# Kernel tuning notes

Hardware: AMD Instinct MI355X
Metric: run time of the kernel (lower is better)

The kernel has to match this reference:

```python
import jax, jax.numpy as jnp
import numpy as np

HIDDEN = 1024
JOINTS = 21
IN_DIM = JOINTS * 3  # 63
BATCH = 64
SEQ = 512


def setup_inputs() -> dict:
    key = jax.random.key(0)
    ks = jax.random.split(key, 11)
    s = 0.02
    f32 = jnp.float32
    return {
        "real_seq": jax.random.normal(ks[0], (BATCH, SEQ, IN_DIM), f32),
        # PyTorch nn.GRU params (gates ordered r, z, n)
        "W_ih": jax.random.normal(ks[1], (3 * HIDDEN, IN_DIM), f32) * s,
        "W_hh": jax.random.normal(ks[2], (3 * HIDDEN, HIDDEN), f32) * s,
        "b_ih": jax.random.normal(ks[3], (3 * HIDDEN,), f32) * s,
        "b_hh": jax.random.normal(ks[4], (3 * HIDDEN,), f32) * s,
        # projector MLP (no nonlinearities in the original)
        "W1": jax.random.normal(ks[5], (HIDDEN, HIDDEN), f32) * s,
        "b1": jax.random.normal(ks[6], (HIDDEN,), f32) * s,
        "W2": jax.random.normal(ks[7], (HIDDEN, HIDDEN), f32) * s,
        "b2": jax.random.normal(ks[8], (HIDDEN,), f32) * s,
        "W3": jax.random.normal(ks[9], (IN_DIM, HIDDEN), f32) * s,
        "b3": jax.random.normal(ks[10], (IN_DIM,), f32) * s,
        "condition_length": 5,
        "ground_truth_length": 5,
    }


def _condition_list(seq_len, condition_length, ground_truth_length):
    gt = np.ones((100, ground_truth_length))
    co = np.zeros((100, condition_length))
    return np.concatenate((gt, co), 1).reshape(-1)[:seq_len]


def reference(real_seq, W_ih, W_hh, b_ih, b_hh, W1, b1, W2, b2, W3, b3,
              condition_length, ground_truth_length):
    B, T, D = real_seq.shape
    H = W_hh.shape[1]
    cond = jnp.asarray(_condition_list(T, condition_length, ground_truth_length),
                       dtype=real_seq.dtype)  # [T], static 1/0 teacher-forcing pattern

    h0 = jnp.zeros((B, H), real_seq.dtype)
    o0 = jnp.zeros((B, D), real_seq.dtype)
    xs = (jnp.transpose(real_seq, (1, 0, 2)), cond)  # time-major

    def step(carry, x):
        h, out = carry
        xt, c = x
        inp = jnp.where(c > 0.5, xt, out)  # teacher-forcing switch
        gi = inp @ W_ih.T + b_ih           # [B, 3H]
        gh = h @ W_hh.T + b_hh             # [B, 3H]
        i_r, i_z, i_n = jnp.split(gi, 3, axis=-1)
        h_r, h_z, h_n = jnp.split(gh, 3, axis=-1)
        r = jax.nn.sigmoid(i_r + h_r)
        z = jax.nn.sigmoid(i_z + h_z)
        n = jnp.tanh(i_n + r * h_n)
        h_new = (1.0 - z) * n + z * h
        lin = (h_new @ W1.T + b1) @ W2.T + b2
        out_new = inp + lin @ W3.T + b3    # residual velocities
        return (h_new, out_new), out_new

    _, outs = jax.lax.scan(step, (h0, o0), xs)  # outs: [T, B, D]
    return jnp.transpose(outs, (1, 0, 2)).reshape(B, T, D // 3, 3)
```

## Files before the change

kernel.cpp:

```cpp
#include <hip/hip_runtime.h>
#include <hip/hip_bf16.h>


#define HIDDEN 1024
#define INDIM  63
#define TSEQ   512
#define MB     16
#define NGRP   4
#define HWORDS 512

typedef __attribute__((ext_vector_type(8))) short bfrag8;
typedef __attribute__((ext_vector_type(4))) float ffrag4;
typedef unsigned long long ull;

#define MFMA_B16(a, b, c) __builtin_amdgcn_mfma_f32_16x16x32_bf16((a), (b), (c), 0, 0, 0)

__device__ __forceinline__ short f2bf(float x) {
  __hip_bfloat16 b = __float2bfloat16(x);
  return __builtin_bit_cast(short, b);
}
__device__ __forceinline__ float bf2f(short s) {
  unsigned u = ((unsigned)(unsigned short)s) << 16;
  return __builtin_bit_cast(float, u);
}


__global__ void k_t1(const float* __restrict__ W2, const float* __restrict__ b1,
                     const float* __restrict__ b2, float* __restrict__ t1) {
  const int w = threadIdx.x >> 6, lane = threadIdx.x & 63;
  const int o = blockIdx.x * 4 + w;
  if (o >= HIDDEN) return;
  const float* row = W2 + (size_t)o * HIDDEN;
  float s = 0.f;
  for (int k = lane; k < HIDDEN; k += 64) s += row[k] * b1[k];
  for (int off = 32; off; off >>= 1) s += __shfl_down(s, off, 64);
  if (lane == 0) t1[o] = s + b2[o];
}

__global__ void k_bp(const float* __restrict__ W3, const float* __restrict__ t1,
                     const float* __restrict__ b3, float* __restrict__ bp) {
  const int w = threadIdx.x >> 6, lane = threadIdx.x & 63;
  for (int d = w; d < INDIM; d += 4) {
    const float* row = W3 + (size_t)d * HIDDEN;
    float s = 0.f;
    for (int k = lane; k < HIDDEN; k += 64) s += row[k] * t1[k];
    for (int off = 32; off; off >>= 1) s += __shfl_down(s, off, 64);
    if (lane == 0) bp[d] = s + b3[d];
  }
}

__global__ void k_gemm(const float* __restrict__ A, const float* __restrict__ B,
                       float* __restrict__ C, int M, int N, int K) {
  __shared__ float As[16][17], Bs[16][17];
  const int tx = threadIdx.x, ty = threadIdx.y;
  const int row = blockIdx.y * 16 + ty;
  const int col = blockIdx.x * 16 + tx;
  float acc = 0.f;
  for (int k0 = 0; k0 < K; k0 += 16) {
    As[ty][tx] = (row < M) ? A[(size_t)row * K + k0 + tx] : 0.f;
    Bs[ty][tx] = B[(size_t)(k0 + ty) * N + col];
    __syncthreads();
#pragma unroll
    for (int kk = 0; kk < 16; ++kk) acc += As[ty][kk] * Bs[kk][tx];
    __syncthreads();
  }
  if (row < M && col < N) C[(size_t)row * N + col] = acc;
}


__global__ __launch_bounds__(256, 1) void k_main(
    const float* __restrict__ X,
    const float* __restrict__ W_ih, const float* __restrict__ W_hh,
    const float* __restrict__ b_ih, const float* __restrict__ b_hh,
    const float* __restrict__ WpF, const float* __restrict__ bpF,
    const int* __restrict__ pCL, const int* __restrict__ pGT,
    ull* __restrict__ hb, float* __restrict__ OUT) {
  __shared__ short h_st[MB][HIDDEN + 8];
  __shared__ short inp_bf[MB][88];
  __shared__ float inp_f[MB][68];
  __shared__ float gt_z[MB][16], gt_hn[MB][16];
  __shared__ float gt_ir[MB][16], gt_iz[MB][16], gt_in[MB][16];
  __shared__ short htmp[MB][16];
  __shared__ int pub_flag;

  const int tid = threadIdx.x;
  const int w = tid >> 6;
  const int lane = tid & 63;
  const int c = lane & 15;
  const int quad = lane >> 4;
  const int g = blockIdx.x >> 6;
  const int j = blockIdx.x & 63;

  const int gtv = pGT[0];
  int period = pCL[0] + gtv;
  if (period < 1) period = 1;

  bfrag8 wB[32];
  bfrag8 wp[32];
  if (w < 3) {
    const float* wr = W_hh + ((size_t)w * HIDDEN + (size_t)j * 16 + c) * HIDDEN;
#pragma unroll
    for (int ks = 0; ks < 32; ++ks) {
      const float* p = wr + ks * 32 + quad * 8;
      bfrag8 f;
#pragma unroll
      for (int e = 0; e < 8; ++e) f[e] = f2bf(p[e]);
      wB[ks] = f;
    }
  } else {
#pragma unroll
    for (int gate = 0; gate < 3; ++gate) {
      const float* wr = W_ih + ((size_t)gate * HIDDEN + (size_t)j * 16 + c) * INDIM;
#pragma unroll
      for (int ks = 0; ks < 2; ++ks) {
        bfrag8 f;
#pragma unroll
        for (int e = 0; e < 8; ++e) {
          int k = ks * 32 + quad * 8 + e;
          f[e] = (k < INDIM) ? f2bf(wr[k]) : (short)0;
        }
        wB[gate * 2 + ks] = f;
      }
    }
  }
  const int dd = 16 * w + c;
  {
    const float* wr = WpF + (size_t)dd * HIDDEN;
#pragma unroll
    for (int ks = 0; ks < 32; ++ks) {
      bfrag8 f;
#pragma unroll
      for (int e = 0; e < 8; ++e)
        f[e] = (dd < INDIM) ? f2bf(wr[ks * 32 + quad * 8 + e]) : (short)0;
      wp[ks] = f;
    }
  }

  float bias_g;
  if (w == 0)      bias_g = b_ih[j * 16 + c] + b_hh[j * 16 + c];
  else if (w == 1) bias_g = b_ih[HIDDEN + j * 16 + c] + b_hh[HIDDEN + j * 16 + c];
  else if (w == 2) bias_g = b_hh[2 * HIDDEN + j * 16 + c];
  else             bias_g = b_ih[2 * HIDDEN + j * 16 + c];
  const float bp_l = (dd < INDIM) ? bpF[dd] : 0.f;

  for (int i = tid; i < MB * (HIDDEN + 8); i += 256) ((short*)h_st)[i] = 0;
  for (int i = tid; i < MB * 88; i += 256) ((short*)inp_bf)[i] = 0;
  for (int i = tid; i < MB * 68; i += 256) ((float*)inp_f)[i] = 0.f;
  if (tid == 0) pub_flag = 0;

  ull* hb_g[2] = {hb + (size_t)g * MB * HWORDS,
                  hb + (size_t)(NGRP + g) * MB * HWORDS};

  for (int t = 0; t < TSEQ; ++t) {
    const unsigned tg = (unsigned)(t + 1);
    const bool teach = ((t % period) < gtv);
    if (teach) {
      const int row = tid >> 4, d0 = (tid & 15) * 4;
      const float* xr = X + ((size_t)(g * MB + row) * TSEQ + t) * INDIM;
#pragma unroll
      for (int e = 0; e < 4; ++e) {
        int d = d0 + e;
        float v = (d < INDIM) ? xr[d] : 0.f;
        inp_f[row][d] = v;
        inp_bf[row][d] = f2bf(v);
      }
    }
    __syncthreads();

    ffrag4 ghr;
    float hp[4];
    if (w < 3) {
      ffrag4 acc[4];
#pragma unroll
      for (int e = 0; e < 4; ++e) {
        acc[0][e] = bias_g; acc[1][e] = 0.f; acc[2][e] = 0.f; acc[3][e] = 0.f;
      }
#pragma unroll
      for (int ks = 0; ks < 32; ++ks) {
        const bfrag8 a = *(const bfrag8*)&h_st[c][ks * 32 + quad * 8];
        acc[ks & 3] = MFMA_B16(a, wB[ks], acc[ks & 3]);
      }
      ffrag4 gsum = acc[0] + acc[1] + acc[2] + acc[3];
      if (w == 1) {
#pragma unroll
        for (int i = 0; i < 4; ++i) gt_z[quad * 4 + i][c] = gsum[i];
      } else if (w == 2) {
#pragma unroll
        for (int i = 0; i < 4; ++i) gt_hn[quad * 4 + i][c] = gsum[i];
      } else {
        ghr = gsum;
#pragma unroll
        for (int i = 0; i < 4; ++i) hp[i] = bf2f(h_st[quad * 4 + i][j * 16 + c]);
      }
    } else {
      ffrag4 gir, giz, gin;
#pragma unroll
      for (int e = 0; e < 4; ++e) { gir[e] = 0.f; giz[e] = 0.f; gin[e] = bias_g; }
#pragma unroll
      for (int ks = 0; ks < 2; ++ks) {
        const bfrag8 a = *(const bfrag8*)&inp_bf[c][ks * 32 + quad * 8];
        gir = MFMA_B16(a, wB[0 + ks], gir);
        giz = MFMA_B16(a, wB[2 + ks], giz);
        gin = MFMA_B16(a, wB[4 + ks], gin);
      }
#pragma unroll
      for (int i = 0; i < 4; ++i) {
        gt_ir[quad * 4 + i][c] = gir[i];
        gt_iz[quad * 4 + i][c] = giz[i];
        gt_in[quad * 4 + i][c] = gin[i];
      }
    }
    __syncthreads();

    ull* hw = hb_g[t & 1];
    if (w == 0) {
#pragma unroll
      for (int i = 0; i < 4; ++i) {
        const int row = quad * 4 + i;
        float r = 1.f / (1.f + __expf(-(ghr[i] + gt_ir[row][c])));
        float z = 1.f / (1.f + __expf(-(gt_z[row][c] + gt_iz[row][c])));
        float n = tanhf(gt_in[row][c] + r * gt_hn[row][c]);
        htmp[row][c] = f2bf((1.f - z) * n + z * hp[i]);
      }
      asm volatile("" ::: "memory");
      const int r = lane >> 2, q4 = (lane & 3) * 4;
      unsigned lo0 = (unsigned)(unsigned short)htmp[r][q4 + 0] |
                     ((unsigned)(unsigned short)htmp[r][q4 + 1] << 16);
      unsigned lo1 = (unsigned)(unsigned short)htmp[r][q4 + 2] |
                     ((unsigned)(unsigned short)htmp[r][q4 + 3] << 16);
      ull w0v = ((ull)tg << 32) | lo0;
      ull w1v = ((ull)tg << 32) | lo1;
      ull* dst = hw + (size_t)r * HWORDS + 8 * j + (lane & 3) * 2;
      __hip_atomic_store(dst, w0v, __ATOMIC_RELAXED, __HIP_MEMORY_SCOPE_SYSTEM);
      __hip_atomic_store(dst + 1, w1v, __ATOMIC_RELAXED, __HIP_MEMORY_SCOPE_SYSTEM);
      asm volatile("" ::: "memory");
      if (lane == 0) *(volatile int*)&pub_flag = (int)tg;
    } else {
      while (*(volatile int*)&pub_flag < (int)tg) __builtin_amdgcn_s_sleep(1);
    }

    {
      ull v[32];
#pragma unroll
      for (int s = 0; s < 32; ++s)
        v[s] = __hip_atomic_load(&hw[tid + s * 256], __ATOMIC_RELAXED,
                                 __HIP_MEMORY_SCOPE_SYSTEM);
      bool bad = true;
      while (bad) {
        bad = false;
#pragma unroll
        for (int s = 0; s < 32; ++s) {
          if ((unsigned)(v[s] >> 32) != tg) {
            v[s] = __hip_atomic_load(&hw[tid + s * 256], __ATOMIC_RELAXED,
                                     __HIP_MEMORY_SCOPE_SYSTEM);
            bad = true;
          }
        }
      }
#pragma unroll
      for (int s = 0; s < 32; ++s) {
        const int widx = tid + s * 256;
        *(unsigned*)&h_st[widx >> 9][(widx & 511) * 2] = (unsigned)v[s];
      }
    }
    __syncthreads();

    const bool rep = (t + 1 < TSEQ) && !(((t + 1) % period) < gtv);
    if (rep || j == 0) {
      ffrag4 oa0, oa1;
#pragma unroll
      for (int e = 0; e < 4; ++e) { oa0[e] = bp_l; oa1[e] = 0.f; }
#pragma unroll
      for (int ks = 0; ks < 32; ++ks) {
        const bfrag8 a = *(const bfrag8*)&h_st[c][ks * 32 + quad * 8];
        if (ks & 1) oa1 = MFMA_B16(a, wp[ks], oa1);
        else        oa0 = MFMA_B16(a, wp[ks], oa0);
      }
      ffrag4 o = oa0 + oa1;
#pragma unroll
      for (int i = 0; i < 4; ++i) {
        const int row = quad * 4 + i;
        if (dd < INDIM) {
          float val = o[i] + inp_f[row][dd];
          if (j == 0) OUT[((size_t)(g * MB + row) * TSEQ + t) * INDIM + dd] = val;
          if (rep) { inp_f[row][dd] = val; inp_bf[row][dd] = f2bf(val); }
        } else if (rep) {
          inp_bf[row][dd] = 0;
        }
      }
    }
  }
}


extern "C" void kernel_launch(void* const* d_in, const int* in_sizes, int n_in,
                              void* d_out, int out_size, void* d_ws, size_t ws_size,
                              hipStream_t stream) {
  const float* X    = (const float*)d_in[0];
  const float* W_ih = (const float*)d_in[1];
  const float* W_hh = (const float*)d_in[2];
  const float* b_ih = (const float*)d_in[3];
  const float* b_hh = (const float*)d_in[4];
  const float* W1   = (const float*)d_in[5];
  const float* b1   = (const float*)d_in[6];
  const float* W2   = (const float*)d_in[7];
  const float* b2   = (const float*)d_in[8];
  const float* W3   = (const float*)d_in[9];
  const float* b3   = (const float*)d_in[10];
  const int* pCL    = (const int*)d_in[11];
  const int* pGT    = (const int*)d_in[12];
  float* OUT = (float*)d_out;

  char* ws = (char*)d_ws;
  float* bp = (float*)(ws + 1024);
  float* t1 = (float*)(ws + 2048);
  float* Wp = (float*)(ws + 8192);
  float* T2 = (float*)(ws + 270336);
  ull*   hb = (ull*)(ws + 270336);
  if (ws_size < 795 * 1024) return;

  k_t1<<<256, 256, 0, stream>>>(W2, b1, b2, t1);
  k_gemm<<<dim3(64, 4), dim3(16, 16), 0, stream>>>(W3, W2, T2, INDIM, HIDDEN, HIDDEN);
  k_gemm<<<dim3(64, 4), dim3(16, 16), 0, stream>>>(T2, W1, Wp, INDIM, HIDDEN, HIDDEN);
  k_bp<<<1, 256, 0, stream>>>(W3, t1, b3, bp);
  hipMemsetAsync(hb, 0, 2 * NGRP * MB * HWORDS * sizeof(ull), stream);
  k_main<<<256, 256, 0, stream>>>(X, W_ih, W_hh, b_ih, b_hh, Wp, bp, pCL, pGT, hb, OUT);
}
```

Baseline: 3.470 ms.

## Use per-block global ready flags and agent-scope atomics for hidden-state exchange

Swaps the per-step cross-block hidden-state handshake from system-scope tagged atomics to agent-scope ones. Producers now publish a per-block flag in global memory after a vmcnt wait, and consumers poll the group's 64 flags before reading the tagged words. The output-writing block rotates with the timestep instead of always being block 0. LDS scratch arrays are padded to reduce bank conflicts. The intent is to cut polling traffic and coherence cost on the serial recurrence critical path, at the cost of extra flag loads and reliance on relaxed ordering between data and flag stores.

```diff
diff --git a/kernel.cpp b/kernel.cpp
--- a/kernel.cpp
+++ b/kernel.cpp
@@ -74,14 +74,13 @@
     const float* __restrict__ b_ih, const float* __restrict__ b_hh,
     const float* __restrict__ WpF, const float* __restrict__ bpF,
     const int* __restrict__ pCL, const int* __restrict__ pGT,
-    ull* __restrict__ hb, float* __restrict__ OUT) {
+    ull* __restrict__ hb, int* __restrict__ fl, float* __restrict__ OUT) {
   __shared__ short h_st[MB][HIDDEN + 8];
   __shared__ short inp_bf[MB][88];
   __shared__ float inp_f[MB][68];
-  __shared__ float gt_z[MB][16], gt_hn[MB][16];
-  __shared__ float gt_ir[MB][16], gt_iz[MB][16], gt_in[MB][16];
-  __shared__ short htmp[MB][16];
-  __shared__ int pub_flag;
+  __shared__ float gt_z[MB][20], gt_hn[MB][20];
+  __shared__ float gt_ir[MB][20], gt_iz[MB][20], gt_in[MB][20];
+  __shared__ short htmp[MB][20];
 
   const int tid = threadIdx.x;
   const int w = tid >> 6;
@@ -146,10 +145,12 @@
   for (int i = tid; i < MB * (HIDDEN + 8); i += 256) ((short*)h_st)[i] = 0;
   for (int i = tid; i < MB * 88; i += 256) ((short*)inp_bf)[i] = 0;
   for (int i = tid; i < MB * 68; i += 256) ((float*)inp_f)[i] = 0.f;
-  if (tid == 0) pub_flag = 0;
 
   ull* hb_g[2] = {hb + (size_t)g * MB * HWORDS,
                   hb + (size_t)(NGRP + g) * MB * HWORDS};
+  int* fg = fl + g * 64;
+  const int fj1 = tid >> 3;
+  const int fj2 = fj1 + 32;
 
   for (int t = 0; t < TSEQ; ++t) {
     const unsigned tg = (unsigned)(t + 1);
@@ -231,20 +232,27 @@
       ull w0v = ((ull)tg << 32) | lo0;
       ull w1v = ((ull)tg << 32) | lo1;
       ull* dst = hw + (size_t)r * HWORDS + 8 * j + (lane & 3) * 2;
-      __hip_atomic_store(dst, w0v, __ATOMIC_RELAXED, __HIP_MEMORY_SCOPE_SYSTEM);
-      __hip_atomic_store(dst + 1, w1v, __ATOMIC_RELAXED, __HIP_MEMORY_SCOPE_SYSTEM);
-      asm volatile("" ::: "memory");
-      if (lane == 0) *(volatile int*)&pub_flag = (int)tg;
-    } else {
-      while (*(volatile int*)&pub_flag < (int)tg) __builtin_amdgcn_s_sleep(1);
+      __hip_atomic_store(dst, w0v, __ATOMIC_RELAXED, __HIP_MEMORY_SCOPE_AGENT);
+      __hip_atomic_store(dst + 1, w1v, __ATOMIC_RELAXED, __HIP_MEMORY_SCOPE_AGENT);
+      asm volatile("s_waitcnt vmcnt(0)" ::: "memory");
+      if (lane == 0)
+        __hip_atomic_store(&fg[j], (int)tg, __ATOMIC_RELAXED,
+                           __HIP_MEMORY_SCOPE_AGENT);
     }
 
     {
+      while (__hip_atomic_load(&fg[fj1], __ATOMIC_RELAXED,
+                               __HIP_MEMORY_SCOPE_AGENT) < (int)tg)
+        __builtin_amdgcn_s_sleep(1);
+      while (__hip_atomic_load(&fg[fj2], __ATOMIC_RELAXED,
+                               __HIP_MEMORY_SCOPE_AGENT) < (int)tg)
+        __builtin_amdgcn_s_sleep(1);
+
       ull v[32];
 #pragma unroll
       for (int s = 0; s < 32; ++s)
         v[s] = __hip_atomic_load(&hw[tid + s * 256], __ATOMIC_RELAXED,
-                                 __HIP_MEMORY_SCOPE_SYSTEM);
+                                 __HIP_MEMORY_SCOPE_AGENT);
       bool bad = true;
       while (bad) {
         bad = false;
@@ -252,7 +260,7 @@
         for (int s = 0; s < 32; ++s) {
           if ((unsigned)(v[s] >> 32) != tg) {
             v[s] = __hip_atomic_load(&hw[tid + s * 256], __ATOMIC_RELAXED,
-                                     __HIP_MEMORY_SCOPE_SYSTEM);
+                                     __HIP_MEMORY_SCOPE_AGENT);
             bad = true;
           }
         }
@@ -265,8 +273,9 @@
     }
     __syncthreads();
 
+    const int wj = t & 63;
     const bool rep = (t + 1 < TSEQ) && !(((t + 1) % period) < gtv);
-    if (rep || j == 0) {
+    if (rep || j == wj) {
       ffrag4 oa0, oa1;
 #pragma unroll
       for (int e = 0; e < 4; ++e) { oa0[e] = bp_l; oa1[e] = 0.f; }
@@ -282,7 +291,7 @@
         const int row = quad * 4 + i;
         if (dd < INDIM) {
           float val = o[i] + inp_f[row][dd];
-          if (j == 0) OUT[((size_t)(g * MB + row) * TSEQ + t) * INDIM + dd] = val;
+          if (j == wj) OUT[((size_t)(g * MB + row) * TSEQ + t) * INDIM + dd] = val;
           if (rep) { inp_f[row][dd] = val; inp_bf[row][dd] = f2bf(val); }
         } else if (rep) {
           inp_bf[row][dd] = 0;
@@ -317,12 +326,16 @@
   float* Wp = (float*)(ws + 8192);
   float* T2 = (float*)(ws + 270336);
   ull*   hb = (ull*)(ws + 270336);
+  int*   fl = (int*)(ws + 270336 + 2 * NGRP * MB * HWORDS * sizeof(ull));
   if (ws_size < 795 * 1024) return;
 
   k_t1<<<256, 256, 0, stream>>>(W2, b1, b2, t1);
   k_gemm<<<dim3(64, 4), dim3(16, 16), 0, stream>>>(W3, W2, T2, INDIM, HIDDEN, HIDDEN);
   k_gemm<<<dim3(64, 4), dim3(16, 16), 0, stream>>>(T2, W1, Wp, INDIM, HIDDEN, HIDDEN);
   k_bp<<<1, 256, 0, stream>>>(W3, t1, b3, bp);
-  hipMemsetAsync(hb, 0, 2 * NGRP * MB * HWORDS * sizeof(ull), stream);
-  k_main<<<256, 256, 0, stream>>>(X, W_ih, W_hh, b_ih, b_hh, Wp, bp, pCL, pGT, hb, OUT);
-}
+  hipMemsetAsync(hb, 0,
+                 2 * NGRP * MB * HWORDS * sizeof(ull) + NGRP * 64 * sizeof(int),
+                 stream);
+  k_main<<<256, 256, 0, stream>>>(X, W_ih, W_hh, b_ih, b_hh, Wp, bp, pCL, pGT,
+                                  hb, fl, OUT);
+}
```

After: 4.263 ms. 22.9% more time.

## Restructure hidden-state exchange with per-element tags, vector polling, and X prefetch

Applied to the files above, without the earlier changes.

Each published bf16 hidden value now carries its own 16-bit timestep tag in a dword, so consumer blocks poll with 16 wide dwordx4 cache-bypassing loads instead of 32 64-bit atomics. Retries are driven by a wave ballot. The next step's teacher-forcing input X is prefetched into registers while waiting on the exchange, taking that load off the critical path. Output writing rotates across blocks to spread the extra projection work, and the shared gate buffers are padded to reduce LDS bank conflicts. In exchange, the inline-asm loads and manual waitcnt rely on coherence behaviour of sc0/sc1, and the 16-bit tag limits how many steps can be distinguished.

```diff
diff --git a/kernel.cpp b/kernel.cpp
--- a/kernel.cpp
+++ b/kernel.cpp
@@ -7,13 +7,18 @@
 #define TSEQ   512
 #define MB     16
 #define NGRP   4
-#define HWORDS 512
+#define HB_DW  (MB * 1024)
 
 typedef __attribute__((ext_vector_type(8))) short bfrag8;
 typedef __attribute__((ext_vector_type(4))) float ffrag4;
+typedef __attribute__((ext_vector_type(4))) unsigned u32x4;
 typedef unsigned long long ull;
 
 #define MFMA_B16(a, b, c) __builtin_amdgcn_mfma_f32_16x16x32_bf16((a), (b), (c), 0, 0, 0)
+
+#define GLOAD4(dst, ptr) \
+  asm volatile("global_load_dwordx4 %0, %1, off sc0 sc1" \
+               : "=v"(dst) : "v"(ptr) : "memory")
 
 __device__ __forceinline__ short f2bf(float x) {
   __hip_bfloat16 b = __float2bfloat16(x);
@@ -74,13 +79,13 @@
     const float* __restrict__ b_ih, const float* __restrict__ b_hh,
     const float* __restrict__ WpF, const float* __restrict__ bpF,
     const int* __restrict__ pCL, const int* __restrict__ pGT,
-    ull* __restrict__ hb, float* __restrict__ OUT) {
+    unsigned* __restrict__ hb, float* __restrict__ OUT) {
   __shared__ short h_st[MB][HIDDEN + 8];
   __shared__ short inp_bf[MB][88];
   __shared__ float inp_f[MB][68];
-  __shared__ float gt_z[MB][16], gt_hn[MB][16];
-  __shared__ float gt_ir[MB][16], gt_iz[MB][16], gt_in[MB][16];
-  __shared__ short htmp[MB][16];
+  __shared__ float gt_z[MB][20], gt_hn[MB][20];
+  __shared__ float gt_ir[MB][20], gt_iz[MB][20], gt_in[MB][20];
+  __shared__ short htmp[MB][20];
   __shared__ int pub_flag;
 
   const int tid = threadIdx.x;
@@ -148,21 +153,25 @@
   for (int i = tid; i < MB * 68; i += 256) ((float*)inp_f)[i] = 0.f;
   if (tid == 0) pub_flag = 0;
 
-  ull* hb_g[2] = {hb + (size_t)g * MB * HWORDS,
-                  hb + (size_t)(NGRP + g) * MB * HWORDS};
+  unsigned* hb_g[2] = {hb + (size_t)g * HB_DW,
+                       hb + (size_t)(NGRP + g) * HB_DW};
+
+  const int xrow = tid >> 4, xd0 = (tid & 15) * 4;
+  float xp[4];
+  if ((0 % period) < gtv) {
+    const float* xr = X + ((size_t)(g * MB + xrow) * TSEQ + 0) * INDIM;
+#pragma unroll
+    for (int e = 0; e < 4; ++e) xp[e] = (xd0 + e < INDIM) ? xr[xd0 + e] : 0.f;
+  }
 
   for (int t = 0; t < TSEQ; ++t) {
     const unsigned tg = (unsigned)(t + 1);
     const bool teach = ((t % period) < gtv);
     if (teach) {
-      const int row = tid >> 4, d0 = (tid & 15) * 4;
-      const float* xr = X + ((size_t)(g * MB + row) * TSEQ + t) * INDIM;
 #pragma unroll
       for (int e = 0; e < 4; ++e) {
-        int d = d0 + e;
-        float v = (d < INDIM) ? xr[d] : 0.f;
-        inp_f[row][d] = v;
-        inp_bf[row][d] = f2bf(v);
+        inp_f[xrow][xd0 + e] = xp[e];
+        inp_bf[xrow][xd0 + e] = f2bf(xp[e]);
       }
     }
     __syncthreads();
@@ -212,7 +221,7 @@
     }
     __syncthreads();
 
-    ull* hw = hb_g[t & 1];
+    unsigned* hw = hb_g[t & 1];
     if (w == 0) {
 #pragma unroll
       for (int i = 0; i < 4; ++i) {
@@ -224,13 +233,13 @@
       }
       asm volatile("" ::: "memory");
       const int r = lane >> 2, q4 = (lane & 3) * 4;
-      unsigned lo0 = (unsigned)(unsigned short)htmp[r][q4 + 0] |
-                     ((unsigned)(unsigned short)htmp[r][q4 + 1] << 16);
-      unsigned lo1 = (unsigned)(unsigned short)htmp[r][q4 + 2] |
-                     ((unsigned)(unsigned short)htmp[r][q4 + 3] << 16);
-      ull w0v = ((ull)tg << 32) | lo0;
-      ull w1v = ((ull)tg << 32) | lo1;
-      ull* dst = hw + (size_t)r * HWORDS + 8 * j + (lane & 3) * 2;
+      unsigned d0 = ((unsigned)tg << 16) | (unsigned)(unsigned short)htmp[r][q4 + 0];
+      unsigned d1 = ((unsigned)tg << 16) | (unsigned)(unsigned short)htmp[r][q4 + 1];
+      unsigned d2 = ((unsigned)tg << 16) | (unsigned)(unsigned short)htmp[r][q4 + 2];
+      unsigned d3 = ((unsigned)tg << 16) | (unsigned)(unsigned short)htmp[r][q4 + 3];
+      ull w0v = ((ull)d1 << 32) | d0;
+      ull w1v = ((ull)d3 << 32) | d2;
+      ull* dst = (ull*)(hw + (size_t)r * 1024 + 16 * j + q4);
       __hip_atomic_store(dst, w0v, __ATOMIC_RELAXED, __HIP_MEMORY_SCOPE_SYSTEM);
       __hip_atomic_store(dst + 1, w1v, __ATOMIC_RELAXED, __HIP_MEMORY_SCOPE_SYSTEM);
       asm volatile("" ::: "memory");
@@ -240,33 +249,59 @@
     }
 
     {
-      ull v[32];
-#pragma unroll
-      for (int s = 0; s < 32; ++s)
-        v[s] = __hip_atomic_load(&hw[tid + s * 256], __ATOMIC_RELAXED,
-                                 __HIP_MEMORY_SCOPE_SYSTEM);
-      bool bad = true;
-      while (bad) {
-        bad = false;
-#pragma unroll
-        for (int s = 0; s < 32; ++s) {
-          if ((unsigned)(v[s] >> 32) != tg) {
-            v[s] = __hip_atomic_load(&hw[tid + s * 256], __ATOMIC_RELAXED,
-                                     __HIP_MEMORY_SCOPE_SYSTEM);
-            bad = true;
-          }
+      const int tn = t + 1;
+      if (tn < TSEQ && ((tn % period) < gtv)) {
+        const float* xr = X + ((size_t)(g * MB + xrow) * TSEQ + tn) * INDIM;
+#pragma unroll
+        for (int e = 0; e < 4; ++e) xp[e] = (xd0 + e < INDIM) ? xr[xd0 + e] : 0.f;
+      }
+    }
+
+    {
+      u32x4 v[16];
+      const unsigned* gp = hw + (size_t)tid * 4;
+#pragma unroll
+      for (int s = 0; s < 16; ++s) GLOAD4(v[s], gp + s * 1024);
+      asm volatile("s_waitcnt vmcnt(0)" ::: "memory");
+      __builtin_amdgcn_sched_barrier(0);
+
+      unsigned bad = 0;
+#pragma unroll
+      for (int s = 0; s < 16; ++s) {
+        if ((v[s][0] >> 16) != tg || (v[s][1] >> 16) != tg ||
+            (v[s][2] >> 16) != tg || (v[s][3] >> 16) != tg)
+          bad |= (1u << s);
+      }
+      while (__ballot(bad != 0)) {
+#pragma unroll
+        for (int s = 0; s < 16; ++s) {
+          if (__ballot((bad >> s) & 1u)) GLOAD4(v[s], gp + s * 1024);
         }
-      }
-#pragma unroll
-      for (int s = 0; s < 32; ++s) {
-        const int widx = tid + s * 256;
-        *(unsigned*)&h_st[widx >> 9][(widx & 511) * 2] = (unsigned)v[s];
-      }
-    }
-    __syncthreads();
-
+        asm volatile("s_waitcnt vmcnt(0)" ::: "memory");
+        __builtin_amdgcn_sched_barrier(0);
+        bad = 0;
+#pragma unroll
+        for (int s = 0; s < 16; ++s) {
+          if ((v[s][0] >> 16) != tg || (v[s][1] >> 16) != tg ||
+              (v[s][2] >> 16) != tg || (v[s][3] >> 16) != tg)
+            bad |= (1u << s);
+        }
+      }
+#pragma unroll
+      for (int s = 0; s < 16; ++s) {
+        const int ci = tid + s * 256;
+        const int row = ci >> 8;
+        const int cb = (ci & 255) * 4;
+        ull p = (ull)(v[s][0] & 0xFFFFu) | ((ull)(v[s][1] & 0xFFFFu) << 16) |
+                ((ull)(v[s][2] & 0xFFFFu) << 32) | ((ull)(v[s][3] & 0xFFFFu) << 48);
+        *(ull*)&h_st[row][cb] = p;
+      }
+    }
+    __syncthreads();
+
+    const int wj = t & 63;
     const bool rep = (t + 1 < TSEQ) && !(((t + 1) % period) < gtv);
-    if (rep || j == 0) {
+    if (rep || j == wj) {
       ffrag4 oa0, oa1;
 #pragma unroll
       for (int e = 0; e < 4; ++e) { oa0[e] = bp_l; oa1[e] = 0.f; }
@@ -282,7 +317,7 @@
         const int row = quad * 4 + i;
         if (dd < INDIM) {
           float val = o[i] + inp_f[row][dd];
-          if (j == 0) OUT[((size_t)(g * MB + row) * TSEQ + t) * INDIM + dd] = val;
+          if (j == wj) OUT[((size_t)(g * MB + row) * TSEQ + t) * INDIM + dd] = val;
           if (rep) { inp_f[row][dd] = val; inp_bf[row][dd] = f2bf(val); }
         } else if (rep) {
           inp_bf[row][dd] = 0;
@@ -316,13 +351,13 @@
   float* t1 = (float*)(ws + 2048);
   float* Wp = (float*)(ws + 8192);
   float* T2 = (float*)(ws + 270336);
-  ull*   hb = (ull*)(ws + 270336);
+  unsigned* hb = (unsigned*)(ws + 270336);
   if (ws_size < 795 * 1024) return;
 
   k_t1<<<256, 256, 0, stream>>>(W2, b1, b2, t1);
   k_gemm<<<dim3(64, 4), dim3(16, 16), 0, stream>>>(W3, W2, T2, INDIM, HIDDEN, HIDDEN);
   k_gemm<<<dim3(64, 4), dim3(16, 16), 0, stream>>>(T2, W1, Wp, INDIM, HIDDEN, HIDDEN);
   k_bp<<<1, 256, 0, stream>>>(W3, t1, b3, bp);
-  hipMemsetAsync(hb, 0, 2 * NGRP * MB * HWORDS * sizeof(ull), stream);
+  hipMemsetAsync(hb, 0, (size_t)2 * NGRP * HB_DW * sizeof(unsigned), stream);
   k_main<<<256, 256, 0, stream>>>(X, W_ih, W_hh, b_ih, b_hh, Wp, bp, pCL, pGT, hb, OUT);
 }
```

New measurement: 3.354 ms (median of 2 runs). 1.03x faster.
